# Kernel optimization log

Hardware: AMD Instinct MI355X
Metric: run time of the kernel (lower is better)

Reference implementation:

```python
import jax, jax.numpy as jnp
import numpy as np

LN_EPS = 1e-5

def _conv2d(x, w, b, pad):
    # x: [B,C,H,W], w: [O,I,kh,kw] -> [B,O,H,W]
    y = jax.lax.conv_general_dilated(
        x, w, window_strides=(1, 1), padding=[(pad, pad), (pad, pad)],
        dimension_numbers=('NCHW', 'OIHW', 'NCHW'))
    return y + b[None, :, None, None]

def setup_inputs() -> dict:
    key = jax.random.key(0)
    ks = jax.random.split(key, 12)
    B, C, H, W = 4, 256, 64, 64
    D = 64  # inner_projection
    s_in = 1.0 / np.sqrt(C)
    s_d1 = 1.0 / np.sqrt(D)
    s_d3 = 1.0 / np.sqrt(D * 9)
    return {
        'x':     jax.random.normal(ks[0], (B, C, H, W), jnp.float32),
        'w_in':  jax.random.normal(ks[1], (D, C, 1, 1), jnp.float32) * s_in,
        'b_in':  jnp.zeros((D,), jnp.float32),
        'wq':    jax.random.normal(ks[2], (D, D, 3, 3), jnp.float32) * s_d3,
        'bq':    jnp.zeros((D,), jnp.float32),
        'wk':    jax.random.normal(ks[3], (D, D, 3, 3), jnp.float32) * s_d3,
        'bk':    jnp.zeros((D,), jnp.float32),
        'wv':    jax.random.normal(ks[4], (D, D, 3, 3), jnp.float32) * s_d3,
        'bv':    jnp.zeros((D,), jnp.float32),
        'w_out': jax.random.normal(ks[5], (C, D, 1, 1), jnp.float32) * s_d1,
        'b_out': jnp.zeros((C,), jnp.float32),
        'gamma': jax.random.normal(ks[6], (1,), jnp.float32) * 0.1,
        'ln_w':  jnp.ones((C,), jnp.float32),
        'ln_b':  jnp.zeros((C,), jnp.float32),
    }

def _attention(q, k, v):
    # full-pixel attention, NO 1/sqrt(d) scale (matches source)
    B, C, H, W = v.shape
    N = H * W
    qf = q.reshape(B, -1, N)   # [B,d,N]
    kf = k.reshape(B, -1, N)
    vf = v.reshape(B, -1, N)
    energy = jnp.einsum('bci,bcj->bij', qf, kf)      # [B,N,N] = Q^T K
    attn = jax.nn.softmax(energy, axis=-1)
    out = jnp.einsum('bcj,bij->bci', vf, attn)        # V @ attn^T
    return out.reshape(B, C, H, W)

def _layernorm2d(x, w, b):
    # normalize over channel dim per pixel (LayerNorm2d)
    mu = jnp.mean(x, axis=1, keepdims=True)
    var = jnp.var(x, axis=1, keepdims=True)
    xn = (x - mu) * jax.lax.rsqrt(var + LN_EPS)
    return xn * w[None, :, None, None] + b[None, :, None, None]

def reference(x, w_in, b_in, wq, bq, wk, bk, wv, bv, w_out, b_out, gamma, ln_w, ln_b):
    att = _conv2d(x, w_in, b_in, 0)          # inner projection [B,D,H,W]
    q = _conv2d(att, wq, bq, 1)
    k = _conv2d(att, wk, bk, 1)
    v = _conv2d(att, wv, bv, 1)
    att = _attention(q, k, v)
    att = _conv2d(att, w_out, b_out, 0)       # outer projection [B,C,H,W]
    return _layernorm2d(gamma * x + att, ln_w, ln_b)
```

## Files before the change

### kernel.cpp

```cpp
#include <hip/hip_runtime.h>
#include <hip/hip_bf16.h>

#define BB 4
#define CC 256
#define DD 64
#define HH 64
#define WW 64
#define NN 4096
#define NSPLIT 8
#define SM_SHIFT 64.0f

typedef __hip_bfloat16 bf16;
typedef __attribute__((ext_vector_type(8))) short bf16x8;
typedef __attribute__((ext_vector_type(4))) float f32x4;
typedef __attribute__((ext_vector_type(4))) short s16x4;

#define MFMA16(a, b, c) __builtin_amdgcn_mfma_f32_16x16x32_bf16(a, b, c, 0, 0, 0)

static __device__ __forceinline__ float ldin(const void* p, size_t i, bool isb) {
  return isb ? __bfloat162float(((const bf16*)p)[i]) : ((const float*)p)[i];
}
static __device__ __forceinline__ void stout(void* p, size_t i, float v, bool isb) {
  if (isb) ((bf16*)p)[i] = __float2bfloat16(v);
  else     ((float*)p)[i] = v;
}
static __device__ __forceinline__ unsigned pack2(bf16 a, bf16 b) {
  unsigned short ua = *reinterpret_cast<unsigned short*>(&a);
  unsigned short ub = *reinterpret_cast<unsigned short*>(&b);
  return (unsigned)ua | ((unsigned)ub << 16);
}
static __device__ __forceinline__ bool probe_bf16(const unsigned* lnw) {
  return lnw[0] == 0x3F803F80u;
}
static __device__ __forceinline__ void split8(const float* v, bf16x8& h8,
                                              bf16x8& l8) {
  #pragma unroll
  for (int r = 0; r < 8; ++r) {
    bf16 h = __float2bfloat16(v[r]);
    float lo = v[r] - __bfloat162float(h);
    bf16 l = __float2bfloat16(lo);
    h8[r] = *reinterpret_cast<short*>(&h);
    l8[r] = *reinterpret_cast<short*>(&l);
  }
}

__global__ __launch_bounds__(256) void k_conv_in_wt(
    const void* __restrict__ x, const void* __restrict__ w_in,
    const void* __restrict__ bias,
    const void* __restrict__ wq, const void* __restrict__ wk,
    const void* __restrict__ wv, const void* __restrict__ w_out,
    bf16* __restrict__ att_h, bf16* __restrict__ att_l,
    bf16* __restrict__ Wth, bf16* __restrict__ Wtl,
    bf16* __restrict__ Wo_h, bf16* __restrict__ Wo_l,
    const unsigned* __restrict__ lnw) {
  const bool isb = probe_bf16(lnw);
  const int id = blockIdx.x;
  const int t = threadIdx.x;
  if (id >= 512) {
    int u = (id - 512) * 256 + t;
    if (u < 110592) {
      int c3 = u / 36864, rem = u % 36864;
      int tap = rem / 4096, r2 = rem % 4096;
      int oc = r2 >> 6, ic = r2 & 63;
      const void* w = (c3 == 0) ? wq : ((c3 == 1) ? wk : wv);
      float v = ldin(w, (size_t)oc * 576 + ic * 9 + tap, isb);
      bf16 h = __float2bfloat16(v);
      Wth[u] = h;
      Wtl[u] = __float2bfloat16(v - __bfloat162float(h));
    } else {
      int v2 = u - 110592;
      float v = ldin(w_out, v2, isb);
      bf16 h = __float2bfloat16(v);
      Wo_h[v2] = h;
      Wo_l[v2] = __float2bfloat16(v - __bfloat162float(h));
    }
    return;
  }
  __shared__ __align__(16) short Xh[32 * 64];
  __shared__ __align__(16) short Xl[32 * 64];
  const int b = id >> 7, n0 = (id & 127) * 32;
  const int w = t >> 6, lane = t & 63, quad = lane >> 4, l16 = lane & 15;
  const int l7 = l16 & 7;
  const size_t xoff = (size_t)b * CC * NN;
  f32x4 acc[2];
  #pragma unroll
  for (int nt = 0; nt < 2; ++nt)
    #pragma unroll
    for (int r = 0; r < 4; ++r)
      acc[nt][r] = ldin(bias, w * 16 + quad * 4 + r, isb);
  for (int c0 = 0; c0 < CC; c0 += 64) {
    __syncthreads();
    #pragma unroll
    for (int i = 0; i < 4; ++i) {
      int u = t + i * 256;
      int dd = u >> 5, n = u & 31;
      float v0 = ldin(x, xoff + (size_t)(c0 + 2 * dd) * NN + n0 + n, isb);
      float v1 = ldin(x, xoff + (size_t)(c0 + 2 * dd + 1) * NN + n0 + n, isb);
      bf16 h0 = __float2bfloat16(v0), h1 = __float2bfloat16(v1);
      bf16 l0 = __float2bfloat16(v0 - __bfloat162float(h0));
      bf16 l1 = __float2bfloat16(v1 - __bfloat162float(h1));
      int cs = ((dd >> 2) ^ (n & 7)) * 8 + ((2 * dd) & 7);
      *(unsigned*)&Xh[n * 64 + cs] = pack2(h0, h1);
      *(unsigned*)&Xl[n * 64 + cs] = pack2(l0, l1);
    }
    __syncthreads();
    #pragma unroll
    for (int kc = 0; kc < 2; ++kc) {
      size_t woff = (size_t)(w * 16 + l16) * 256 + c0 + kc * 32 + quad * 8;
      bf16x8 wh, wl;
      if (isb) {
        wh = *(const bf16x8*)((const bf16*)w_in + woff);
      } else {
        const float* wp = (const float*)w_in + woff;
        float4 a0 = *(const float4*)wp;
        float4 a1 = *(const float4*)(wp + 4);
        float vv[8] = {a0.x, a0.y, a0.z, a0.w, a1.x, a1.y, a1.z, a1.w};
        split8(vv, wh, wl);
      }
      const int xo = ((kc * 4 + quad) ^ l7) * 8;
      #pragma unroll
      for (int nt = 0; nt < 2; ++nt) {
        int rn = nt * 16 + l16;
        bf16x8 xh = *(const bf16x8*)&Xh[rn * 64 + xo];
        bf16x8 xl = *(const bf16x8*)&Xl[rn * 64 + xo];
        acc[nt] = MFMA16(wh, xh, acc[nt]);
        acc[nt] = MFMA16(wh, xl, acc[nt]);
        if (!isb) acc[nt] = MFMA16(wl, xh, acc[nt]);
      }
    }
  }
  #pragma unroll
  for (int nt = 0; nt < 2; ++nt) {
    size_t off = ((size_t)b * NN + n0 + nt * 16 + l16) * DD + w * 16 + quad * 4;
    bf16 h[4], l[4];
    #pragma unroll
    for (int r = 0; r < 4; ++r) {
      float v = acc[nt][r];
      h[r] = __float2bfloat16(v);
      l[r] = __float2bfloat16(v - __bfloat162float(h[r]));
    }
    *(uint2*)&att_h[off] = make_uint2(pack2(h[0], h[1]), pack2(h[2], h[3]));
    *(uint2*)&att_l[off] = make_uint2(pack2(l[0], l[1]), pack2(l[2], l[3]));
  }
}

__global__ __launch_bounds__(256) void k_conv3(
    const bf16* __restrict__ att_h, const bf16* __restrict__ att_l,
    const bf16* __restrict__ Wth, const bf16* __restrict__ Wtl,
    const void* __restrict__ bq, const void* __restrict__ bk,
    const void* __restrict__ bv,
    bf16* __restrict__ qth, bf16* __restrict__ qtl,
    bf16* __restrict__ kth, bf16* __restrict__ ktl,
    bf16* __restrict__ vt, const unsigned* __restrict__ lnw) {
  __shared__ __align__(16) short Ah[3 * 66 * 64];
  __shared__ __align__(16) short Al[3 * 66 * 64];
  float* o_s = reinterpret_cast<float*>(Ah);
  const bool isb = probe_bf16(lnw);
  const int y = blockIdx.x, b = blockIdx.y, c3 = blockIdx.z;
  const int t = threadIdx.x;
  const int w = t >> 6, lane = t & 63, quad = lane >> 4, l16 = lane & 15;
  const uint4 z4 = make_uint4(0, 0, 0, 0);
  #pragma unroll
  for (int r = 0; r < 3; ++r) {
    int yp = y + r - 1;
    bool ok = (unsigned)yp < 64u;
    const uint4* sh = (const uint4*)(att_h + ((size_t)b * NN + (size_t)yp * 64) * DD);
    const uint4* sl = (const uint4*)(att_l + ((size_t)b * NN + (size_t)yp * 64) * DD);
    #pragma unroll
    for (int ii = 0; ii < 2; ++ii) {
      int u = t + ii * 256;
      int xx = u >> 3, ch = u & 7;
      int rr = r * 66 + xx + 1;
      uint4 vh = ok ? sh[u] : z4;
      uint4 vl = ok ? sl[u] : z4;
      int cs = (ch ^ (rr & 7)) * 8;
      *(uint4*)&Ah[rr * 64 + cs] = vh;
      *(uint4*)&Al[rr * 64 + cs] = vl;
    }
    if (t < 16) {
      int rr = r * 66 + ((t & 1) ? 65 : 0);
      int cs = (t >> 1) * 8;
      *(uint4*)&Ah[rr * 64 + cs] = z4;
      *(uint4*)&Al[rr * 64 + cs] = z4;
    }
  }
  __syncthreads();
  const void* bp = (c3 == 0) ? bq : ((c3 == 1) ? bk : bv);
  const bf16* wth = Wth + (size_t)c3 * 9 * 4096;
  const bf16* wtl = Wtl + (size_t)c3 * 9 * 4096;
  f32x4 acc[4];
  #pragma unroll
  for (int nt = 0; nt < 4; ++nt)
    #pragma unroll
    for (int r = 0; r < 4; ++r)
      acc[nt][r] = ldin(bp, w * 16 + quad * 4 + r, isb);
  #pragma unroll
  for (int tap = 0; tap < 9; ++tap) {
    const int dy = tap / 3, dx = tap % 3;
    const int woff = tap * 4096 + (w * 16 + l16) * 64 + quad * 8;
    bf16x8 wh0 = *(const bf16x8*)(wth + woff);
    bf16x8 wh1 = *(const bf16x8*)(wth + woff + 32);
    bf16x8 wl0 = *(const bf16x8*)(wtl + woff);
    bf16x8 wl1 = *(const bf16x8*)(wtl + woff + 32);
    #pragma unroll
    for (int nt = 0; nt < 4; ++nt) {
      int rr = dy * 66 + nt * 16 + l16 + dx;
      int chA = (quad ^ (rr & 7)) * 8;
      int chB = ((quad + 4) ^ (rr & 7)) * 8;
      bf16x8 ah0 = *(const bf16x8*)&Ah[rr * 64 + chA];
      bf16x8 ah1 = *(const bf16x8*)&Ah[rr * 64 + chB];
      bf16x8 al0 = *(const bf16x8*)&Al[rr * 64 + chA];
      bf16x8 al1 = *(const bf16x8*)&Al[rr * 64 + chB];
      acc[nt] = MFMA16(wh0, ah0, acc[nt]);
      acc[nt] = MFMA16(wh1, ah1, acc[nt]);
      acc[nt] = MFMA16(wh0, al0, acc[nt]);
      acc[nt] = MFMA16(wh1, al1, acc[nt]);
      acc[nt] = MFMA16(wl0, ah0, acc[nt]);
      acc[nt] = MFMA16(wl1, ah1, acc[nt]);
    }
  }
  if (c3 < 2) {
    bf16* dh = (c3 == 0) ? qth : kth;
    bf16* dl = (c3 == 0) ? qtl : ktl;
    const size_t rowb = (size_t)b * NN + (size_t)y * 64;
    #pragma unroll
    for (int nt = 0; nt < 4; ++nt) {
      size_t off = (rowb + nt * 16 + l16) * DD + w * 16 + quad * 4;
      bf16 h[4], l[4];
      #pragma unroll
      for (int r = 0; r < 4; ++r) {
        float v = acc[nt][r];
        h[r] = __float2bfloat16(v);
        l[r] = __float2bfloat16(v - __bfloat162float(h[r]));
      }
      *(uint2*)&dh[off] = make_uint2(pack2(h[0], h[1]), pack2(h[2], h[3]));
      *(uint2*)&dl[off] = make_uint2(pack2(l[0], l[1]), pack2(l[2], l[3]));
    }
  } else {
    __syncthreads();
    #pragma unroll
    for (int nt = 0; nt < 4; ++nt)
      #pragma unroll
      for (int r = 0; r < 4; ++r)
        o_s[(nt * 16 + l16) * 65 + w * 16 + quad * 4 + r] = acc[nt][r];
    __syncthreads();
    #pragma unroll
    for (int i = 0; i < 8; ++i) {
      int u = t + i * 256;
      int c = u >> 5, np = (u & 31) * 2;
      float v0 = o_s[np * 65 + c], v1 = o_s[(np + 1) * 65 + c];
      *(unsigned*)&vt[((size_t)b * DD + c) * NN + (size_t)y * 64 + np] =
          pack2(__float2bfloat16(v0), __float2bfloat16(v1));
    }
  }
}

__global__ __launch_bounds__(256) void k_attn(
    const bf16* __restrict__ qth, const bf16* __restrict__ qtl,
    const bf16* __restrict__ kth, const bf16* __restrict__ ktl,
    const bf16* __restrict__ vt, bf16* __restrict__ po,
    float* __restrict__ pl) {
  __shared__ __align__(16) short Kh[64 * 64];
  __shared__ __align__(16) short Kl[64 * 64];
  __shared__ __align__(16) short Vs[64 * 64];
  __shared__ __align__(16) short Ps[64 * 64];
  const int b = blockIdx.y, i0 = blockIdx.x * 64, sp = blockIdx.z;
  const int jt0 = sp * (64 / NSPLIT), jt1 = jt0 + (64 / NSPLIT);
  const int t = threadIdx.x;
  const int w = t >> 6, lane = t & 63, quad = lane >> 4, l16 = lane & 15;
  const int l7 = l16 & 7;
  const int xA = (quad ^ l7) * 8;
  const int xB = ((quad + 4) ^ l7) * 8;
  const int sr = t >> 2, m4 = t & 3, sg = m4 * 16;
  const int sc0 = ((2 * m4) ^ (sr & 7)) * 8;
  const int sc1 = ((2 * m4 + 1) ^ (sr & 7)) * 8;
  {
    size_t off = ((size_t)b * NN + i0 + sr) * DD + sg;
    const uint4* qh = (const uint4*)(qth + off);
    const uint4* ql = (const uint4*)(qtl + off);
    *(uint4*)&Kh[sr * 64 + sc0] = qh[0];
    *(uint4*)&Kh[sr * 64 + sc1] = qh[1];
    *(uint4*)&Kl[sr * 64 + sc0] = ql[0];
    *(uint4*)&Kl[sr * 64 + sc1] = ql[1];
  }
  uint4 kh0, kh1, kl0, kl1, vx0, vx1;
  {
    size_t koff = ((size_t)b * NN + jt0 * 64 + sr) * DD + sg;
    kh0 = ((const uint4*)(kth + koff))[0]; kh1 = ((const uint4*)(kth + koff))[1];
    kl0 = ((const uint4*)(ktl + koff))[0]; kl1 = ((const uint4*)(ktl + koff))[1];
    size_t voff = ((size_t)b * DD + sr) * NN + jt0 * 64 + sg;
    vx0 = ((const uint4*)(vt + voff))[0];  vx1 = ((const uint4*)(vt + voff))[1];
  }
  __syncthreads();
  const int rq = w * 16 + l16;
  const bf16x8 qf_h0 = *(const bf16x8*)&Kh[rq * 64 + xA];
  const bf16x8 qf_h1 = *(const bf16x8*)&Kh[rq * 64 + xB];
  const bf16x8 qf_l0 = *(const bf16x8*)&Kl[rq * 64 + xA];
  const bf16x8 qf_l1 = *(const bf16x8*)&Kl[rq * 64 + xB];
  float l_run = 0.f;
  f32x4 oacc[4] = {};
  for (int jt = jt0; jt < jt1; ++jt) {
    __syncthreads();
    *(uint4*)&Kh[sr * 64 + sc0] = kh0;    *(uint4*)&Kh[sr * 64 + sc1] = kh1;
    *(uint4*)&Kl[sr * 64 + sc0] = kl0;    *(uint4*)&Kl[sr * 64 + sc1] = kl1;
    *(uint4*)&Vs[sr * 64 + sc0] = vx0;    *(uint4*)&Vs[sr * 64 + sc1] = vx1;
    __syncthreads();
    if (jt < jt1 - 1) {
      int j0n = (jt + 1) * 64;
      size_t koff = ((size_t)b * NN + j0n + sr) * DD + sg;
      kh0 = ((const uint4*)(kth + koff))[0]; kh1 = ((const uint4*)(kth + koff))[1];
      kl0 = ((const uint4*)(ktl + koff))[0]; kl1 = ((const uint4*)(ktl + koff))[1];
      size_t voff = ((size_t)b * DD + sr) * NN + j0n + sg;
      vx0 = ((const uint4*)(vt + voff))[0];  vx1 = ((const uint4*)(vt + voff))[1];
    }
    f32x4 s[4];
    #pragma unroll
    for (int mt = 0; mt < 4; ++mt) {
      int r0 = (mt * 16 + l16) * 64;
      bf16x8 kf_h0 = *(const bf16x8*)&Kh[r0 + xA];
      bf16x8 kf_h1 = *(const bf16x8*)&Kh[r0 + xB];
      bf16x8 kf_l0 = *(const bf16x8*)&Kl[r0 + xA];
      bf16x8 kf_l1 = *(const bf16x8*)&Kl[r0 + xB];
      f32x4 c = {0.f, 0.f, 0.f, 0.f};
      c = MFMA16(kf_h0, qf_h0, c);
      c = MFMA16(kf_h1, qf_h1, c);
      c = MFMA16(kf_h0, qf_l0, c);
      c = MFMA16(kf_h1, qf_l1, c);
      c = MFMA16(kf_l0, qf_h0, c);
      c = MFMA16(kf_l1, qf_h1, c);
      s[mt] = c;
    }
    float psum = 0.f;
    short pb[16];
    #pragma unroll
    for (int mt = 0; mt < 4; ++mt)
      #pragma unroll
      for (int r = 0; r < 4; ++r) {
        float p = __expf(s[mt][r] - SM_SHIFT);
        bf16 ph = __float2bfloat16(p);
        psum += __bfloat162float(ph);
        pb[mt * 4 + r] = *reinterpret_cast<short*>(&ph);
      }
    psum += __shfl_xor(psum, 16, 64);
    psum += __shfl_xor(psum, 32, 64);
    l_run += psum;
    #pragma unroll
    for (int mt = 0; mt < 4; ++mt) {
      s16x4 pk;
      pk.x = pb[mt * 4 + 0]; pk.y = pb[mt * 4 + 1];
      pk.z = pb[mt * 4 + 2]; pk.w = pb[mt * 4 + 3];
      int chP = ((2 * mt + (quad >> 1)) ^ l7) * 8 + (quad & 1) * 4;
      *(s16x4*)&Ps[rq * 64 + chP] = pk;
    }
    bf16x8 pf0 = *(const bf16x8*)&Ps[rq * 64 + xA];
    bf16x8 pf1 = *(const bf16x8*)&Ps[rq * 64 + xB];
    #pragma unroll
    for (int mt = 0; mt < 4; ++mt) {
      int r0 = (mt * 16 + l16) * 64;
      bf16x8 vf0 = *(const bf16x8*)&Vs[r0 + xA];
      bf16x8 vf1 = *(const bf16x8*)&Vs[r0 + xB];
      oacc[mt] = MFMA16(vf0, pf0, oacc[mt]);
      oacc[mt] = MFMA16(vf1, pf1, oacc[mt]);
    }
  }
  const int ig = i0 + w * 16 + l16;
  const size_t SEGC = (size_t)BB * DD * NN;
  #pragma unroll
  for (int mt = 0; mt < 4; ++mt)
    #pragma unroll
    for (int r = 0; r < 4; ++r) {
      int c = mt * 16 + quad * 4 + r;
      po[(size_t)sp * SEGC + ((size_t)b * DD + c) * NN + ig] =
          __float2bfloat16(oacc[mt][r]);
    }
  if (quad == 0) pl[((size_t)sp * BB + b) * NN + ig] = l_run;
}

__global__ __launch_bounds__(256) void k_out_ln(
    const bf16* __restrict__ po, const float* __restrict__ pl,
    const void* __restrict__ x,
    const bf16* __restrict__ Wo_h, const bf16* __restrict__ Wo_l,
    const void* __restrict__ bias, const void* __restrict__ gamma,
    const void* __restrict__ lw, const void* __restrict__ lb,
    void* __restrict__ out, const unsigned* __restrict__ lnw) {
  __shared__ __align__(16) short Ahs[16 * 64];
  __shared__ __align__(16) short Als[16 * 64];
  __shared__ float inv_s[16];
  __shared__ float red1[16 * 4], red2[16 * 4];
  __shared__ float mu_s[16], rs_s[16];
  __shared__ float lw_s[256], lb_s[256];
  const bool isb = probe_bf16(lnw);
  const int b = blockIdx.y, n0 = blockIdx.x * 16;
  const int t = threadIdx.x;
  const int w = t >> 6, lane = t & 63, quad = lane >> 4, l16 = lane & 15;
  const int l7 = l16 & 7;
  const size_t SEGC = (size_t)BB * DD * NN;
  if (t < 16) {
    int i = n0 + t;
    float lsum = 0.f;
    #pragma unroll
    for (int s = 0; s < NSPLIT; ++s) lsum += pl[((size_t)s * BB + b) * NN + i];
    inv_s[t] = 1.f / lsum;
  }
  lw_s[t] = ldin(lw, t, isb);
  lb_s[t] = ldin(lb, t, isb);
  const float g = ldin(gamma, 0, isb);
  __syncthreads();
  #pragma unroll
  for (int i = 0; i < 2; ++i) {
    int u = t + i * 256;
    int dd = u >> 4, n = u & 15;
    size_t base = ((size_t)b * DD + 2 * dd) * NN + n0 + n;
    float v0 = 0.f, v1 = 0.f;
    #pragma unroll
    for (int s = 0; s < NSPLIT; ++s) {
      v0 += __bfloat162float(po[(size_t)s * SEGC + base]);
      v1 += __bfloat162float(po[(size_t)s * SEGC + base + NN]);
    }
    float inv = inv_s[n];
    v0 *= inv; v1 *= inv;
    bf16 h0 = __float2bfloat16(v0), h1 = __float2bfloat16(v1);
    bf16 l0 = __float2bfloat16(v0 - __bfloat162float(h0));
    bf16 l1 = __float2bfloat16(v1 - __bfloat162float(h1));
    int cs = ((dd >> 2) ^ (n & 7)) * 8 + ((2 * dd) & 7);
    *(unsigned*)&Ahs[n * 64 + cs] = pack2(h0, h1);
    *(unsigned*)&Als[n * 64 + cs] = pack2(l0, l1);
  }
  f32x4 acc[4];
  #pragma unroll
  for (int oct = 0; oct < 4; ++oct)
    #pragma unroll
    for (int r = 0; r < 4; ++r)
      acc[oct][r] = ldin(bias, w * 64 + oct * 16 + quad * 4 + r, isb);
  __syncthreads();
  #pragma unroll
  for (int oct = 0; oct < 4; ++oct) {
    const int base = w * 64 + oct * 16;
    #pragma unroll
    for (int kc = 0; kc < 2; ++kc) {
      size_t woff = (size_t)(base + l16) * 64 + kc * 32 + quad * 8;
      bf16x8 wh = *(const bf16x8*)(Wo_h + woff);
      bf16x8 wl = *(const bf16x8*)(Wo_l + woff);
      const int xo = ((kc * 4 + quad) ^ l7) * 8;
      bf16x8 ah = *(const bf16x8*)&Ahs[l16 * 64 + xo];
      bf16x8 al = *(const bf16x8*)&Als[l16 * 64 + xo];
      acc[oct] = MFMA16(wh, ah, acc[oct]);
      acc[oct] = MFMA16(wh, al, acc[oct]);
      acc[oct] = MFMA16(wl, ah, acc[oct]);
    }
  }
  {
    int nn = l16;
    float s1 = 0.f, s2 = 0.f;
    #pragma unroll
    for (int oct = 0; oct < 4; ++oct)
      #pragma unroll
      for (int r = 0; r < 4; ++r) {
        int oc = w * 64 + oct * 16 + quad * 4 + r;
        float xv = ldin(x, ((size_t)b * CC + oc) * NN + n0 + nn, isb);
        float y = acc[oct][r] + g * xv;
        acc[oct][r] = y;
        s1 += y; s2 += y * y;
      }
    s1 += __shfl_xor(s1, 16, 64); s1 += __shfl_xor(s1, 32, 64);
    s2 += __shfl_xor(s2, 16, 64); s2 += __shfl_xor(s2, 32, 64);
    if (quad == 0) { red1[nn * 4 + w] = s1; red2[nn * 4 + w] = s2; }
  }
  __syncthreads();
  if (t < 16) {
    float sm = red1[t * 4] + red1[t * 4 + 1] + red1[t * 4 + 2] + red1[t * 4 + 3];
    float sq = red2[t * 4] + red2[t * 4 + 1] + red2[t * 4 + 2] + red2[t * 4 + 3];
    float mu = sm * (1.f / 256.f);
    float var = sq * (1.f / 256.f) - mu * mu;
    mu_s[t] = mu;
    rs_s[t] = rsqrtf(var + 1e-5f);
  }
  __syncthreads();
  {
    int nn = l16;
    float mu = mu_s[nn], rs = rs_s[nn];
    #pragma unroll
    for (int oct = 0; oct < 4; ++oct)
      #pragma unroll
      for (int r = 0; r < 4; ++r) {
        int oc = w * 64 + oct * 16 + quad * 4 + r;
        float o = (acc[oct][r] - mu) * rs * lw_s[oc] + lb_s[oc];
        stout(out, ((size_t)b * CC + oc) * NN + n0 + nn, o, isb);
      }
  }
}

extern "C" void kernel_launch(void* const* d_in, const int* in_sizes, int n_in,
                              void* d_out, int out_size, void* d_ws, size_t ws_size,
                              hipStream_t stream) {
  const void* x     = d_in[0];
  const void* w_in  = d_in[1];
  const void* b_in  = d_in[2];
  const void* wq    = d_in[3];
  const void* bq    = d_in[4];
  const void* wk    = d_in[5];
  const void* bk    = d_in[6];
  const void* wv    = d_in[7];
  const void* bv    = d_in[8];
  const void* w_out = d_in[9];
  const void* b_out = d_in[10];
  const void* gamma = d_in[11];
  const void* ln_w  = d_in[12];
  const void* ln_b  = d_in[13];

  const size_t SEG = (size_t)BB * DD * NN;
  char*  p     = (char*)d_ws;
  bf16*  att_h = (bf16*)p;  p += SEG * 2;
  bf16*  att_l = (bf16*)p;  p += SEG * 2;
  bf16*  qth   = (bf16*)p;  p += SEG * 2;
  bf16*  qtl   = (bf16*)p;  p += SEG * 2;
  bf16*  kth   = (bf16*)p;  p += SEG * 2;
  bf16*  ktl   = (bf16*)p;  p += SEG * 2;
  bf16*  vt    = (bf16*)p;  p += SEG * 2;
  bf16*  po    = (bf16*)p;  p += (size_t)NSPLIT * SEG * 2;
  float* pl    = (float*)p; p += (size_t)NSPLIT * BB * NN * 4;
  bf16*  Wth   = (bf16*)p;  p += 110592 * 2;
  bf16*  Wtl   = (bf16*)p;  p += 110592 * 2;
  bf16*  Wo_h  = (bf16*)p;  p += 16384 * 2;
  bf16*  Wo_l  = (bf16*)p;  p += 16384 * 2;
  const unsigned* lnw = (const unsigned*)ln_w;

  k_conv_in_wt<<<1008, 256, 0, stream>>>(x, w_in, b_in, wq, wk, wv, w_out,
                                         att_h, att_l, Wth, Wtl, Wo_h, Wo_l,
                                         lnw);
  k_conv3<<<dim3(64, BB, 3), 256, 0, stream>>>(att_h, att_l, Wth, Wtl,
                                               bq, bk, bv,
                                               qth, qtl, kth, ktl, vt, lnw);
  k_attn<<<dim3(NN / 64, BB, NSPLIT), 256, 0, stream>>>(qth, qtl, kth, ktl, vt,
                                                        po, pl);
  k_out_ln<<<dim3(NN / 16, BB), 256, 0, stream>>>(po, pl, x, Wo_h, Wo_l,
                                                  b_out, gamma, ln_w, ln_b,
                                                  d_out, lnw);
}
```

Baseline: 190.4 us.

## Split conv3 rows into half-row tiles and widen out_ln pixel tiles

The 3x3 conv kernel now tiles each image row into two 32-pixel halves, doubling its grid to 1536 blocks and halving the per-block shared memory so more blocks fit per CU. The output projection plus layernorm kernel now processes 32 pixels per block instead of 16, reusing each loaded weight fragment across two MFMA tiles and halving its grid. The conv change trades extra halo loads for parallelism and occupancy. The out_ln change trades block count and register pressure for weight reuse.

```diff
diff --git a/kernel.cpp b/kernel.cpp
--- a/kernel.cpp
+++ b/kernel.cpp
@@ -152,45 +152,39 @@
     bf16* __restrict__ qth, bf16* __restrict__ qtl,
     bf16* __restrict__ kth, bf16* __restrict__ ktl,
     bf16* __restrict__ vt, const unsigned* __restrict__ lnw) {
-  __shared__ __align__(16) short Ah[3 * 66 * 64];
-  __shared__ __align__(16) short Al[3 * 66 * 64];
+  __shared__ __align__(16) short Ah[3 * 34 * 64];
+  __shared__ __align__(16) short Al[3 * 34 * 64];
   float* o_s = reinterpret_cast<float*>(Ah);
   const bool isb = probe_bf16(lnw);
-  const int y = blockIdx.x, b = blockIdx.y, c3 = blockIdx.z;
+  const int y = blockIdx.x >> 1, x0 = (blockIdx.x & 1) * 32;
+  const int b = blockIdx.y, c3 = blockIdx.z;
   const int t = threadIdx.x;
   const int w = t >> 6, lane = t & 63, quad = lane >> 4, l16 = lane & 15;
   const uint4 z4 = make_uint4(0, 0, 0, 0);
   #pragma unroll
-  for (int r = 0; r < 3; ++r) {
-    int yp = y + r - 1;
-    bool ok = (unsigned)yp < 64u;
-    const uint4* sh = (const uint4*)(att_h + ((size_t)b * NN + (size_t)yp * 64) * DD);
-    const uint4* sl = (const uint4*)(att_l + ((size_t)b * NN + (size_t)yp * 64) * DD);
-    #pragma unroll
-    for (int ii = 0; ii < 2; ++ii) {
-      int u = t + ii * 256;
-      int xx = u >> 3, ch = u & 7;
-      int rr = r * 66 + xx + 1;
-      uint4 vh = ok ? sh[u] : z4;
-      uint4 vl = ok ? sl[u] : z4;
-      int cs = (ch ^ (rr & 7)) * 8;
-      *(uint4*)&Ah[rr * 64 + cs] = vh;
-      *(uint4*)&Al[rr * 64 + cs] = vl;
-    }
-    if (t < 16) {
-      int rr = r * 66 + ((t & 1) ? 65 : 0);
-      int cs = (t >> 1) * 8;
-      *(uint4*)&Ah[rr * 64 + cs] = z4;
-      *(uint4*)&Al[rr * 64 + cs] = z4;
+  for (int i = 0; i < 4; ++i) {
+    int u = t + i * 256;
+    if (u < 816) {
+      int r = u / 272, rem = u % 272;
+      int xx = rem >> 3, ch = rem & 7;
+      int yp = y + r - 1, gx = x0 - 1 + xx;
+      bool ok = ((unsigned)yp < 64u) && ((unsigned)gx < 64u);
+      size_t gi = ((size_t)b * NN + (size_t)yp * 64 + gx) * 8 + ch;
+      uint4 vh = ok ? ((const uint4*)att_h)[gi] : z4;
+      uint4 vl = ok ? ((const uint4*)att_l)[gi] : z4;
+      int rl = r * 34 + xx;
+      int cs = (ch ^ (rl & 7)) * 8;
+      *(uint4*)&Ah[rl * 64 + cs] = vh;
+      *(uint4*)&Al[rl * 64 + cs] = vl;
     }
   }
   __syncthreads();
   const void* bp = (c3 == 0) ? bq : ((c3 == 1) ? bk : bv);
   const bf16* wth = Wth + (size_t)c3 * 9 * 4096;
   const bf16* wtl = Wtl + (size_t)c3 * 9 * 4096;
-  f32x4 acc[4];
-  #pragma unroll
-  for (int nt = 0; nt < 4; ++nt)
+  f32x4 acc[2];
+  #pragma unroll
+  for (int nt = 0; nt < 2; ++nt)
     #pragma unroll
     for (int r = 0; r < 4; ++r)
       acc[nt][r] = ldin(bp, w * 16 + quad * 4 + r, isb);
@@ -203,8 +197,8 @@
     bf16x8 wl0 = *(const bf16x8*)(wtl + woff);
     bf16x8 wl1 = *(const bf16x8*)(wtl + woff + 32);
     #pragma unroll
-    for (int nt = 0; nt < 4; ++nt) {
-      int rr = dy * 66 + nt * 16 + l16 + dx;
+    for (int nt = 0; nt < 2; ++nt) {
+      int rr = dy * 34 + nt * 16 + l16 + dx;
       int chA = (quad ^ (rr & 7)) * 8;
       int chB = ((quad + 4) ^ (rr & 7)) * 8;
       bf16x8 ah0 = *(const bf16x8*)&Ah[rr * 64 + chA];
@@ -222,9 +216,9 @@
   if (c3 < 2) {
     bf16* dh = (c3 == 0) ? qth : kth;
     bf16* dl = (c3 == 0) ? qtl : ktl;
-    const size_t rowb = (size_t)b * NN + (size_t)y * 64;
-    #pragma unroll
-    for (int nt = 0; nt < 4; ++nt) {
+    const size_t rowb = (size_t)b * NN + (size_t)y * 64 + x0;
+    #pragma unroll
+    for (int nt = 0; nt < 2; ++nt) {
       size_t off = (rowb + nt * 16 + l16) * DD + w * 16 + quad * 4;
       bf16 h[4], l[4];
       #pragma unroll
@@ -239,17 +233,17 @@
   } else {
     __syncthreads();
     #pragma unroll
-    for (int nt = 0; nt < 4; ++nt)
+    for (int nt = 0; nt < 2; ++nt)
       #pragma unroll
       for (int r = 0; r < 4; ++r)
         o_s[(nt * 16 + l16) * 65 + w * 16 + quad * 4 + r] = acc[nt][r];
     __syncthreads();
     #pragma unroll
-    for (int i = 0; i < 8; ++i) {
+    for (int i = 0; i < 4; ++i) {
       int u = t + i * 256;
-      int c = u >> 5, np = (u & 31) * 2;
+      int c = u >> 4, np = (u & 15) * 2;
       float v0 = o_s[np * 65 + c], v1 = o_s[(np + 1) * 65 + c];
-      *(unsigned*)&vt[((size_t)b * DD + c) * NN + (size_t)y * 64 + np] =
+      *(unsigned*)&vt[((size_t)b * DD + c) * NN + (size_t)y * 64 + x0 + np] =
           pack2(__float2bfloat16(v0), __float2bfloat16(v1));
     }
   }
@@ -383,19 +377,19 @@
     const void* __restrict__ bias, const void* __restrict__ gamma,
     const void* __restrict__ lw, const void* __restrict__ lb,
     void* __restrict__ out, const unsigned* __restrict__ lnw) {
-  __shared__ __align__(16) short Ahs[16 * 64];
-  __shared__ __align__(16) short Als[16 * 64];
-  __shared__ float inv_s[16];
-  __shared__ float red1[16 * 4], red2[16 * 4];
-  __shared__ float mu_s[16], rs_s[16];
+  __shared__ __align__(16) short Ahs[32 * 64];
+  __shared__ __align__(16) short Als[32 * 64];
+  __shared__ float inv_s[32];
+  __shared__ float red1[32 * 4], red2[32 * 4];
+  __shared__ float mu_s[32], rs_s[32];
   __shared__ float lw_s[256], lb_s[256];
   const bool isb = probe_bf16(lnw);
-  const int b = blockIdx.y, n0 = blockIdx.x * 16;
+  const int b = blockIdx.y, n0 = blockIdx.x * 32;
   const int t = threadIdx.x;
   const int w = t >> 6, lane = t & 63, quad = lane >> 4, l16 = lane & 15;
   const int l7 = l16 & 7;
   const size_t SEGC = (size_t)BB * DD * NN;
-  if (t < 16) {
+  if (t < 32) {
     int i = n0 + t;
     float lsum = 0.f;
     #pragma unroll
@@ -407,9 +401,9 @@
   const float g = ldin(gamma, 0, isb);
   __syncthreads();
   #pragma unroll
-  for (int i = 0; i < 2; ++i) {
+  for (int i = 0; i < 4; ++i) {
     int u = t + i * 256;
-    int dd = u >> 4, n = u & 15;
+    int dd = u >> 5, n = u & 31;
     size_t base = ((size_t)b * DD + 2 * dd) * NN + n0 + n;
     float v0 = 0.f, v1 = 0.f;
     #pragma unroll
@@ -426,12 +420,15 @@
     *(unsigned*)&Ahs[n * 64 + cs] = pack2(h0, h1);
     *(unsigned*)&Als[n * 64 + cs] = pack2(l0, l1);
   }
-  f32x4 acc[4];
+  f32x4 acc[4][2];
   #pragma unroll
   for (int oct = 0; oct < 4; ++oct)
     #pragma unroll
-    for (int r = 0; r < 4; ++r)
-      acc[oct][r] = ldin(bias, w * 64 + oct * 16 + quad * 4 + r, isb);
+    for (int r = 0; r < 4; ++r) {
+      float bo = ldin(bias, w * 64 + oct * 16 + quad * 4 + r, isb);
+      #pragma unroll
+      for (int nt = 0; nt < 2; ++nt) acc[oct][nt][r] = bo;
+    }
   __syncthreads();
   #pragma unroll
   for (int oct = 0; oct < 4; ++oct) {
@@ -442,15 +439,20 @@
       bf16x8 wh = *(const bf16x8*)(Wo_h + woff);
       bf16x8 wl = *(const bf16x8*)(Wo_l + woff);
       const int xo = ((kc * 4 + quad) ^ l7) * 8;
-      bf16x8 ah = *(const bf16x8*)&Ahs[l16 * 64 + xo];
-      bf16x8 al = *(const bf16x8*)&Als[l16 * 64 + xo];
-      acc[oct] = MFMA16(wh, ah, acc[oct]);
-      acc[oct] = MFMA16(wh, al, acc[oct]);
-      acc[oct] = MFMA16(wl, ah, acc[oct]);
-    }
-  }
-  {
-    int nn = l16;
+      #pragma unroll
+      for (int nt = 0; nt < 2; ++nt) {
+        int rn = nt * 16 + l16;
+        bf16x8 ah = *(const bf16x8*)&Ahs[rn * 64 + xo];
+        bf16x8 al = *(const bf16x8*)&Als[rn * 64 + xo];
+        acc[oct][nt] = MFMA16(wh, ah, acc[oct][nt]);
+        acc[oct][nt] = MFMA16(wh, al, acc[oct][nt]);
+        acc[oct][nt] = MFMA16(wl, ah, acc[oct][nt]);
+      }
+    }
+  }
+  #pragma unroll
+  for (int nt = 0; nt < 2; ++nt) {
+    int nn = nt * 16 + l16;
     float s1 = 0.f, s2 = 0.f;
     #pragma unroll
     for (int oct = 0; oct < 4; ++oct)
@@ -458,8 +460,8 @@
       for (int r = 0; r < 4; ++r) {
         int oc = w * 64 + oct * 16 + quad * 4 + r;
         float xv = ldin(x, ((size_t)b * CC + oc) * NN + n0 + nn, isb);
-        float y = acc[oct][r] + g * xv;
-        acc[oct][r] = y;
+        float y = acc[oct][nt][r] + g * xv;
+        acc[oct][nt][r] = y;
         s1 += y; s2 += y * y;
       }
     s1 += __shfl_xor(s1, 16, 64); s1 += __shfl_xor(s1, 32, 64);
@@ -467,7 +469,7 @@
     if (quad == 0) { red1[nn * 4 + w] = s1; red2[nn * 4 + w] = s2; }
   }
   __syncthreads();
-  if (t < 16) {
+  if (t < 32) {
     float sm = red1[t * 4] + red1[t * 4 + 1] + red1[t * 4 + 2] + red1[t * 4 + 3];
     float sq = red2[t * 4] + red2[t * 4 + 1] + red2[t * 4 + 2] + red2[t * 4 + 3];
     float mu = sm * (1.f / 256.f);
@@ -476,15 +478,16 @@
     rs_s[t] = rsqrtf(var + 1e-5f);
   }
   __syncthreads();
-  {
-    int nn = l16;
+  #pragma unroll
+  for (int nt = 0; nt < 2; ++nt) {
+    int nn = nt * 16 + l16;
     float mu = mu_s[nn], rs = rs_s[nn];
     #pragma unroll
     for (int oct = 0; oct < 4; ++oct)
       #pragma unroll
       for (int r = 0; r < 4; ++r) {
         int oc = w * 64 + oct * 16 + quad * 4 + r;
-        float o = (acc[oct][r] - mu) * rs * lw_s[oc] + lb_s[oc];
+        float o = (acc[oct][nt][r] - mu) * rs * lw_s[oc] + lb_s[oc];
         stout(out, ((size_t)b * CC + oc) * NN + n0 + nn, o, isb);
       }
   }
@@ -528,12 +531,12 @@
   k_conv_in_wt<<<1008, 256, 0, stream>>>(x, w_in, b_in, wq, wk, wv, w_out,
                                          att_h, att_l, Wth, Wtl, Wo_h, Wo_l,
                                          lnw);
-  k_conv3<<<dim3(64, BB, 3), 256, 0, stream>>>(att_h, att_l, Wth, Wtl,
-                                               bq, bk, bv,
-                                               qth, qtl, kth, ktl, vt, lnw);
+  k_conv3<<<dim3(128, BB, 3), 256, 0, stream>>>(att_h, att_l, Wth, Wtl,
+                                                bq, bk, bv,
+                                                qth, qtl, kth, ktl, vt, lnw);
   k_attn<<<dim3(NN / 64, BB, NSPLIT), 256, 0, stream>>>(qth, qtl, kth, ktl, vt,
                                                         po, pl);
-  k_out_ln<<<dim3(NN / 16, BB), 256, 0, stream>>>(po, pl, x, Wo_h, Wo_l,
+  k_out_ln<<<dim3(NN / 32, BB), 256, 0, stream>>>(po, pl, x, Wo_h, Wo_l,
                                                   b_out, gamma, ln_w, ln_b,
                                                   d_out, lnw);
 }
```

Measured after the change: 196.6 us. +3.3%, slower.
